# Kernel optimization log

Measured on AMD Instinct MI355X. Metric: run time of the kernel, lower is better.

The kernel has to match this reference:

```python
import jax, jax.numpy as jnp
import numpy as np

D_MODEL = 1024
H = 16
D_K = D_MODEL // H
D_FF = 4096
EPS = 1e-6


def layer_norm(x, alpha, bias):
    mean = jnp.mean(x, axis=-1, keepdims=True)
    var = jnp.mean((x - mean) ** 2, axis=-1, keepdims=True)  # unbiased=False
    return alpha * (x - mean) / jnp.sqrt(var + EPS) + bias


def setup_inputs() -> dict:
    key = jax.random.key(0)
    ks = jax.random.split(key, 8)
    B, S = 4, 2048
    sd = 1.0 / np.sqrt(D_MODEL)
    x = jax.random.normal(ks[0], (B, S, D_MODEL), dtype=jnp.float32)
    src_mask = jnp.ones((B, 1, S), dtype=jnp.int32)
    wq = jax.random.normal(ks[1], (D_MODEL, D_MODEL), jnp.float32) * sd
    wk = jax.random.normal(ks[2], (D_MODEL, D_MODEL), jnp.float32) * sd
    wv = jax.random.normal(ks[3], (D_MODEL, D_MODEL), jnp.float32) * sd
    wo = jax.random.normal(ks[4], (D_MODEL, D_MODEL), jnp.float32) * sd
    w1 = jax.random.normal(ks[5], (D_FF, D_MODEL), jnp.float32) * sd
    b1 = jnp.zeros((D_FF,), jnp.float32)
    w2 = jax.random.normal(ks[6], (D_MODEL, D_FF), jnp.float32) * (1.0 / np.sqrt(D_FF))
    b2 = jnp.zeros((D_MODEL,), jnp.float32)
    ln1_a = jnp.ones((D_MODEL,), jnp.float32)
    ln1_b = jnp.zeros((D_MODEL,), jnp.float32)
    ln2_a = jnp.ones((D_MODEL,), jnp.float32)
    ln2_b = jnp.zeros((D_MODEL,), jnp.float32)
    return dict(x=x, src_mask=src_mask, wq=wq, wk=wk, wv=wv, wo=wo,
                ln1_a=ln1_a, ln1_b=ln1_b, ln2_a=ln2_a, ln2_b=ln2_b,
                w1=w1, b1=b1, w2=w2, b2=b2)


def attention(xn, wq, wk, wv, wo, src_mask):
    B, S, _ = xn.shape
    # torch nn.Linear: y = x @ W.T
    q = (xn @ wq.T).reshape(B, S, H, D_K).transpose(0, 2, 1, 3)  # [B,H,S,Dk]
    k = (xn @ wk.T).reshape(B, S, H, D_K).transpose(0, 2, 1, 3)
    v = (xn @ wv.T).reshape(B, S, H, D_K).transpose(0, 2, 1, 3)
    scores = jnp.einsum('bhqd,bhkd->bhqk', q, k) / np.sqrt(D_K)
    m = src_mask[:, None, :, :]  # [B,1,1,S] from [B,1,S]
    scores = jnp.where(m == 0, -jnp.inf, scores)
    attn = jax.nn.softmax(scores, axis=-1)
    out = jnp.einsum('bhqk,bhkd->bhqd', attn, v)
    out = out.transpose(0, 2, 1, 3).reshape(B, S, D_MODEL)
    return out @ wo.T


def reference(x, src_mask, wq, wk, wv, wo, ln1_a, ln1_b, ln2_a, ln2_b, w1, b1, w2, b2):
    # pre-LN residual 1: self-attention
    xn = layer_norm(x, ln1_a, ln1_b)
    x = x + attention(xn, wq, wk, wv, wo, src_mask)
    # pre-LN residual 2: FFN
    xn = layer_norm(x, ln2_a, ln2_b)
    h = jax.nn.relu(xn @ w1.T + b1)
    x = x + (h @ w2.T + b2)
    return x
```

## Files before the change

### kernel.cpp

```cpp
#include <hip/hip_runtime.h>
#include <stdint.h>

typedef unsigned short u16;
typedef __bf16 bf16x8 __attribute__((ext_vector_type(8)));
typedef float   f32x4 __attribute__((ext_vector_type(4)));
typedef u16     u16x8 __attribute__((ext_vector_type(8)));
typedef u16     u16x4 __attribute__((ext_vector_type(4)));

__device__ __forceinline__ float bf2f(u16 u) {
    union { uint32_t i; float f; } c; c.i = ((uint32_t)u) << 16; return c.f;
}
__device__ __forceinline__ u16 f2bf(float f) {
    union { float f; uint32_t i; } c; c.f = f;
    uint32_t r = c.i + 0x7FFFu + ((c.i >> 16) & 1u);
    return (u16)(r >> 16);
}
__device__ __forceinline__ u16 f2bf_fast(float f) {
    union { float f; uint32_t i; } c; c.f = f;
    return (u16)((c.i + 0x8000u) >> 16);
}
__device__ __forceinline__ uint32_t cvt_pk_bf16(float lo, float hi) {
    uint32_t r;
    asm("v_cvt_pk_bf16_f32 %0, %1, %2" : "=v"(r) : "v"(lo), "v"(hi));
    return r;
}
__device__ __forceinline__ void gload_lds16(const u16* g, u16* l) {
    __builtin_amdgcn_global_load_lds(
        (__attribute__((address_space(1))) void*)(g),
        (__attribute__((address_space(3))) void*)(l), 16, 0, 0);
}

__global__ __launch_bounds__(256) void cvt_all(
    const float* __restrict__ wq, const float* __restrict__ wk,
    const float* __restrict__ wv, const float* __restrict__ wo,
    const float* __restrict__ w1, const float* __restrict__ w2,
    u16* __restrict__ wqb, u16* __restrict__ wkb, u16* __restrict__ wvb,
    u16* __restrict__ wob, u16* __restrict__ w1b, u16* __restrict__ w2b)
{
    int blk = blockIdx.x;
    const float* src; u16* dst; int off;
    if      (blk < 1024)  { src = wq; dst = wqb; off = blk; }
    else if (blk < 2048)  { src = wk; dst = wkb; off = blk - 1024; }
    else if (blk < 3072)  { src = wv; dst = wvb; off = blk - 2048; }
    else if (blk < 4096)  { src = wo; dst = wob; off = blk - 3072; }
    else if (blk < 8192)  { src = w1; dst = w1b; off = blk - 4096; }
    else                  { src = w2; dst = w2b; off = blk - 8192; }
    int i = off * 1024 + threadIdx.x * 4;
    float4 v = *(const float4*)(src + i);
    u16x4 o; o[0] = f2bf(v.x); o[1] = f2bf(v.y); o[2] = f2bf(v.z); o[3] = f2bf(v.w);
    *(u16x4*)(dst + i) = o;
}

__global__ __launch_bounds__(256) void ln_kernel(
    const float* __restrict__ x, const float* __restrict__ ga,
    const float* __restrict__ be, u16* __restrict__ out)
{
    const int D = 1024;
    int row  = blockIdx.x * 4 + (threadIdx.x >> 6);
    int lane = threadIdx.x & 63;
    const float* xr = x + (size_t)row * D + lane * 16;
    float f[16];
#pragma unroll
    for (int i = 0; i < 4; ++i) *(float4*)&f[i * 4] = *(const float4*)(xr + i * 4);
    float s = 0.f, s2 = 0.f;
#pragma unroll
    for (int i = 0; i < 16; ++i) { s += f[i]; s2 += f[i] * f[i]; }
#pragma unroll
    for (int off = 1; off < 64; off <<= 1) {
        s  += __shfl_xor(s,  off, 64);
        s2 += __shfl_xor(s2, off, 64);
    }
    float mean = s * (1.0f / 1024.0f);
    float var  = s2 * (1.0f / 1024.0f) - mean * mean;
    var = var < 0.f ? 0.f : var;
    float inv = 1.0f / sqrtf(var + 1e-6f);
    float g[16], b[16];
#pragma unroll
    for (int i = 0; i < 4; ++i) {
        *(float4*)&g[i * 4] = *(const float4*)(ga + lane * 16 + i * 4);
        *(float4*)&b[i * 4] = *(const float4*)(be + lane * 16 + i * 4);
    }
    u16x8 o0, o1;
#pragma unroll
    for (int i = 0; i < 8; ++i) {
        o0[i] = f2bf(g[i]     * (f[i]     - mean) * inv + b[i]);
        o1[i] = f2bf(g[8 + i] * (f[8 + i] - mean) * inv + b[8 + i]);
    }
    u16* orow = out + (size_t)row * D + lane * 16;
    *(u16x8*)(orow)     = o0;
    *(u16x8*)(orow + 8) = o1;
}

__device__ __forceinline__ void gemm_core(
    const u16* __restrict__ A, const u16* __restrict__ W,
    int K, int ldw, int row_a0, int row_w0,
    u16* As, u16* Bs, f32x4 (&acc)[4][4])
{
    int tid  = threadIdx.x;
    int lane = tid & 63;
    int quad = (lane >> 4), l16 = lane & 15;
    int wave = tid >> 6;
    int wr = wave >> 1, wc = wave & 1;
    int srow = tid >> 2, scol = (tid & 3) * 8;
    const u16* a0p = A + (size_t)(row_a0 + srow) * K + scol;
    const u16* a1p = a0p + (size_t)64 * K;
    const u16* b0p = W + (size_t)(row_w0 + srow) * ldw + scol;
    const u16* b1p = b0p + (size_t)64 * ldw;
    u16* la0 = As + tid * 8;
    u16* la1 = As + 2048 + tid * 8;
    u16* la2 = As + 4096 + tid * 8;
    u16* la3 = As + 6144 + tid * 8;
    u16* lb0 = Bs + tid * 8;
    u16* lb1 = Bs + 2048 + tid * 8;
    u16* lb2 = Bs + 4096 + tid * 8;
    u16* lb3 = Bs + 6144 + tid * 8;

    for (int k0 = 0; k0 < K; k0 += 64) {
        __syncthreads();
        gload_lds16(a0p + k0,      la0);
        gload_lds16(a1p + k0,      la1);
        gload_lds16(a0p + k0 + 32, la2);
        gload_lds16(a1p + k0 + 32, la3);
        gload_lds16(b0p + k0,      lb0);
        gload_lds16(b1p + k0,      lb1);
        gload_lds16(b0p + k0 + 32, lb2);
        gload_lds16(b1p + k0 + 32, lb3);
        __syncthreads();
#pragma unroll
        for (int h = 0; h < 2; ++h) {
            const u16* Ah = As + h * 4096;
            const u16* Bh = Bs + h * 4096;
            bf16x8 af[4], bf[4];
#pragma unroll
            for (int mt = 0; mt < 4; ++mt)
                af[mt] = *(const bf16x8*)(&Ah[(wr * 64 + mt * 16 + l16) * 32 + quad * 8]);
#pragma unroll
            for (int nt = 0; nt < 4; ++nt)
                bf[nt] = *(const bf16x8*)(&Bh[(wc * 64 + nt * 16 + l16) * 32 + quad * 8]);
#pragma unroll
            for (int mt = 0; mt < 4; ++mt)
#pragma unroll
                for (int nt = 0; nt < 4; ++nt)
                    acc[mt][nt] = __builtin_amdgcn_mfma_f32_16x16x32_bf16(
                        af[mt], bf[nt], acc[mt][nt], 0, 0, 0);
        }
    }
}

template<bool OUTF32>
__global__ __launch_bounds__(256) void gemm128(
    const u16* __restrict__ A, const u16* __restrict__ W,
    const float* __restrict__ bias, const float* __restrict__ resid,
    void* __restrict__ Cp, int M, int N, int K, int ldw, int do_relu)
{
    __shared__ u16 As[128 * 64];
    __shared__ u16 Bs[128 * 64];
    int tid  = threadIdx.x;
    int lane = tid & 63, wave = tid >> 6;
    int quad = lane >> 4, l16 = lane & 15;
    int wr = wave >> 1, wc = wave & 1;
    const int row_a0 = blockIdx.x * 128, row_w0 = blockIdx.y * 128;
    f32x4 acc[4][4] = {};
    gemm_core(A, W, K, ldw, row_a0, row_w0, As, Bs, acc);
#pragma unroll
    for (int mt = 0; mt < 4; ++mt) {
#pragma unroll
        for (int nt = 0; nt < 4; ++nt) {
#pragma unroll
            for (int r = 0; r < 4; ++r) {
                int grow = row_a0 + wr * 64 + mt * 16 + quad * 4 + r;
                int gcol = row_w0 + wc * 64 + nt * 16 + l16;
                float vv = acc[mt][nt][r];
                if (bias)    vv += bias[gcol];
                if (do_relu) vv = vv > 0.f ? vv : 0.f;
                if (resid)   vv += resid[(size_t)grow * N + gcol];
                if (OUTF32) ((float*)Cp)[(size_t)grow * N + gcol] = vv;
                else        ((u16*)Cp)[(size_t)grow * N + gcol] = f2bf(vv);
            }
        }
    }
}

__global__ __launch_bounds__(256) void gemm128_qkv(
    const u16* __restrict__ A, const u16* __restrict__ Wqkv,
    u16* __restrict__ qo, u16* __restrict__ ko, u16* __restrict__ vo, int K)
{
    __shared__ u16 As[128 * 64];
    __shared__ u16 Bs[128 * 64];
    int tid  = threadIdx.x;
    int lane = tid & 63, wave = tid >> 6;
    int quad = lane >> 4, l16 = lane & 15;
    int wr = wave >> 1, wc = wave & 1;
    const int row_a0 = blockIdx.x * 128, row_w0 = blockIdx.y * 128;
    f32x4 acc[4][4] = {};
    gemm_core(A, Wqkv, K, K, row_a0, row_w0, As, Bs, acc);
    int seg = row_w0 >> 10;
    u16* dst = (seg == 0) ? qo : (seg == 1) ? ko : vo;
    int col0 = row_w0 & 1023;
#pragma unroll
    for (int mt = 0; mt < 4; ++mt) {
#pragma unroll
        for (int nt = 0; nt < 4; ++nt) {
#pragma unroll
            for (int r = 0; r < 4; ++r) {
                int grow = row_a0 + wr * 64 + mt * 16 + quad * 4 + r;
                int gcol = col0 + wc * 64 + nt * 16 + l16;
                dst[(size_t)grow * 1024 + gcol] = f2bf(acc[mt][nt][r]);
            }
        }
    }
}

__global__ __launch_bounds__(512, 4) void attn_kernel(
    const u16* __restrict__ Q, const u16* __restrict__ Km, const u16* __restrict__ Vm,
    const int* __restrict__ mask, u16* __restrict__ O)
{
    const int S = 2048, DM = 1024;
    const float C1 = 0.18033688f;
    const float C0 = -11.541560f;
    __shared__ u16 smem[35840];
    u16* Ks0 = smem;
    u16* Ks1 = smem + 4096;
    u16* Vt0 = smem + 8192;
    u16* Vt1 = smem + 12800;
    u16* Ps  = smem + 17408;
    u16* Qs  = smem + 17408;

    int qt = blockIdx.x, bh = blockIdx.y;
    int b = bh >> 4, h = bh & 15;
    int tid = threadIdx.x;
    int wave = tid >> 6, lane = tid & 63;
    int quad = lane >> 4, l16 = lane & 15;
    size_t base = (size_t)b * S;
    size_t hoff = (size_t)h * 64;

    {
        int r = tid >> 1, c0 = (tid & 1) * 32;
        const u16* src = Q + (base + qt * 256 + r) * DM + hoff + c0;
        u16* dq = Qs + r * 72 + c0;
        *(u16x8*)(dq)      = *(const u16x8*)(src);
        *(u16x8*)(dq + 8)  = *(const u16x8*)(src + 8);
        *(u16x8*)(dq + 16) = *(const u16x8*)(src + 16);
        *(u16x8*)(dq + 24) = *(const u16x8*)(src + 24);
    }
    const u16* ksrc = Km + (base + (tid >> 3)) * DM + hoff
                    + ((tid & 7) ^ ((tid >> 5) & 7)) * 8;
    int kp = tid & 31, d0 = (tid >> 5) * 4;
    const u16* vsrc = Vm + (base + kp * 2) * DM + hoff + d0;
    const int* msrc = mask + b * S + 4 * l16;

    __syncthreads();
    const int q0 = wave * 32;
    bf16x8 qf00 = *(const bf16x8*)(&Qs[(q0 + l16) * 72 + quad * 8]);
    bf16x8 qf01 = *(const bf16x8*)(&Qs[(q0 + l16) * 72 + 32 + quad * 8]);
    bf16x8 qf10 = *(const bf16x8*)(&Qs[(q0 + 16 + l16) * 72 + quad * 8]);
    bf16x8 qf11 = *(const bf16x8*)(&Qs[(q0 + 16 + l16) * 72 + 32 + quad * 8]);
    const int swz = (l16 & 7) * 8;
    const int u0  = (quad * 8) ^ swz;

    {
        u16x4 va = *(const u16x4*)(vsrc);
        u16x4 vb = *(const u16x4*)(vsrc + DM);
        gload_lds16(ksrc, Ks0 + tid * 8);
        ksrc += 64 * DM; vsrc += 64 * DM;
#pragma unroll
        for (int i = 0; i < 4; ++i) {
            uint32_t w = (uint32_t)va[i] | ((uint32_t)vb[i] << 16);
            *(uint32_t*)(&Vt0[(d0 + i) * 72 + kp * 2]) = w;
        }
    }
    __syncthreads();

    float l0[4] = {0.f, 0.f, 0.f, 0.f};
    float l1[4] = {0.f, 0.f, 0.f, 0.f};
    f32x4 o0[4] = {}, o1[4] = {};

    for (int it = 0; it < 32; ++it) {
        const u16* Kcur = (it & 1) ? Ks1 : Ks0;
        const u16* Vcur = (it & 1) ? Vt1 : Vt0;
        u16* Knxt = (it & 1) ? Ks0 : Ks1;
        u16* Vnxt = (it & 1) ? Vt0 : Vt1;
        const bool pfch = (it < 31);
        u16x4 va, vb;
        if (pfch) {
            va = *(const u16x4*)(vsrc);
            vb = *(const u16x4*)(vsrc + DM);
            gload_lds16(ksrc, Knxt + tid * 8);
            ksrc += 64 * DM; vsrc += 64 * DM;
        }
        f32x4 s0[4] = {}, s1[4] = {};
#pragma unroll
        for (int t = 0; t < 4; ++t) {
            const u16* krp = Kcur + (4 * l16 + t) * 64;
            bf16x8 kf0 = *(const bf16x8*)(krp + u0);
            bf16x8 kf1 = *(const bf16x8*)(krp + (u0 ^ 32));
            s0[t] = __builtin_amdgcn_mfma_f32_16x16x32_bf16(qf00, kf0, s0[t], 0, 0, 0);
            s0[t] = __builtin_amdgcn_mfma_f32_16x16x32_bf16(qf01, kf1, s0[t], 0, 0, 0);
            s1[t] = __builtin_amdgcn_mfma_f32_16x16x32_bf16(qf10, kf0, s1[t], 0, 0, 0);
            s1[t] = __builtin_amdgcn_mfma_f32_16x16x32_bf16(qf11, kf1, s1[t], 0, 0, 0);
        }
        int4 mk4 = *(const int4*)(msrc); msrc += 64;
        float c0t[4];
        c0t[0] = (mk4.x == 0) ? -1e38f : C0;
        c0t[1] = (mk4.y == 0) ? -1e38f : C0;
        c0t[2] = (mk4.z == 0) ? -1e38f : C0;
        c0t[3] = (mk4.w == 0) ? -1e38f : C0;
#pragma unroll
        for (int r = 0; r < 4; ++r) {
            float p0 = exp2f(fmaf(s0[0][r], C1, c0t[0]));
            float p1 = exp2f(fmaf(s0[1][r], C1, c0t[1]));
            float p2 = exp2f(fmaf(s0[2][r], C1, c0t[2]));
            float p3 = exp2f(fmaf(s0[3][r], C1, c0t[3]));
            l0[r] += (p0 + p1) + (p2 + p3);
            uint2 pw;
            pw.x = cvt_pk_bf16(p0, p1);
            pw.y = cvt_pk_bf16(p2, p3);
            *(uint2*)(&Ps[(q0 + quad * 4 + r) * 72 + 4 * l16]) = pw;
        }
#pragma unroll
        for (int r = 0; r < 4; ++r) {
            float p0 = exp2f(fmaf(s1[0][r], C1, c0t[0]));
            float p1 = exp2f(fmaf(s1[1][r], C1, c0t[1]));
            float p2 = exp2f(fmaf(s1[2][r], C1, c0t[2]));
            float p3 = exp2f(fmaf(s1[3][r], C1, c0t[3]));
            l1[r] += (p0 + p1) + (p2 + p3);
            uint2 pw;
            pw.x = cvt_pk_bf16(p0, p1);
            pw.y = cvt_pk_bf16(p2, p3);
            *(uint2*)(&Ps[(q0 + 16 + quad * 4 + r) * 72 + 4 * l16]) = pw;
        }
        bf16x8 pf00 = *(const bf16x8*)(&Ps[(q0 + l16) * 72 + quad * 8]);
        bf16x8 pf01 = *(const bf16x8*)(&Ps[(q0 + l16) * 72 + 32 + quad * 8]);
        bf16x8 pf10 = *(const bf16x8*)(&Ps[(q0 + 16 + l16) * 72 + quad * 8]);
        bf16x8 pf11 = *(const bf16x8*)(&Ps[(q0 + 16 + l16) * 72 + 32 + quad * 8]);
#pragma unroll
        for (int t = 0; t < 4; ++t) {
            bf16x8 vf0 = *(const bf16x8*)(&Vcur[(t * 16 + l16) * 72 + quad * 8]);
            bf16x8 vf1 = *(const bf16x8*)(&Vcur[(t * 16 + l16) * 72 + 32 + quad * 8]);
            o0[t] = __builtin_amdgcn_mfma_f32_16x16x32_bf16(pf00, vf0, o0[t], 0, 0, 0);
            o0[t] = __builtin_amdgcn_mfma_f32_16x16x32_bf16(pf01, vf1, o0[t], 0, 0, 0);
            o1[t] = __builtin_amdgcn_mfma_f32_16x16x32_bf16(pf10, vf0, o1[t], 0, 0, 0);
            o1[t] = __builtin_amdgcn_mfma_f32_16x16x32_bf16(pf11, vf1, o1[t], 0, 0, 0);
        }
        if (pfch) {
#pragma unroll
            for (int i = 0; i < 4; ++i) {
                uint32_t w = (uint32_t)va[i] | ((uint32_t)vb[i] << 16);
                *(uint32_t*)(&Vnxt[(d0 + i) * 72 + kp * 2]) = w;
            }
        }
        __syncthreads();
    }
#pragma unroll
    for (int r = 0; r < 4; ++r) {
#pragma unroll
        for (int off = 1; off < 16; off <<= 1) {
            l0[r] += __shfl_xor(l0[r], off, 16);
            l1[r] += __shfl_xor(l1[r], off, 16);
        }
        float i0 = 1.0f / l0[r];
        float i1 = 1.0f / l1[r];
        u16* dst0 = O + (base + qt * 256 + q0 + quad * 4 + r) * DM + hoff + l16;
        u16* dst1 = dst0 + (size_t)16 * DM;
#pragma unroll
        for (int t = 0; t < 4; ++t) {
            dst0[t * 16] = f2bf(o0[t][r] * i0);
            dst1[t * 16] = f2bf(o1[t][r] * i1);
        }
    }
}

extern "C" void kernel_launch(void* const* d_in, const int* in_sizes, int n_in,
                              void* d_out, int out_size, void* d_ws, size_t ws_size,
                              hipStream_t stream)
{
    (void)in_sizes; (void)n_in; (void)out_size; (void)ws_size;
    const float* x    = (const float*)d_in[0];
    const int*   mask = (const int*)d_in[1];
    const float* wq   = (const float*)d_in[2];
    const float* wk   = (const float*)d_in[3];
    const float* wv   = (const float*)d_in[4];
    const float* wo   = (const float*)d_in[5];
    const float* ln1a = (const float*)d_in[6];
    const float* ln1b = (const float*)d_in[7];
    const float* ln2a = (const float*)d_in[8];
    const float* ln2b = (const float*)d_in[9];
    const float* w1   = (const float*)d_in[10];
    const float* b1   = (const float*)d_in[11];
    const float* w2   = (const float*)d_in[12];
    const float* b2   = (const float*)d_in[13];

    const int M = 8192, D = 1024, F = 4096;
    char* ws = (char*)d_ws;
    u16*  wqkv = (u16*)(ws);
    u16*  wqb = wqkv;
    u16*  wkb = (u16*)(ws + (2u  << 20));
    u16*  wvb = (u16*)(ws + (4u  << 20));
    u16*  wob = (u16*)(ws + (6u  << 20));
    u16*  w1b = (u16*)(ws + (8u  << 20));
    u16*  w2b = (u16*)(ws + (16u << 20));
    u16*  xn  = (u16*)(ws + (24u << 20));
    u16*  q   = (u16*)(ws + (40u << 20));
    u16*  hb  = (u16*)(ws + (40u << 20));

    u16*   kbuf = (u16*)d_out;
    u16*   vbuf = (u16*)d_out + (size_t)M * D;
    float* x1   = (float*)d_out;

    cvt_all<<<12288, 256, 0, stream>>>(wq, wk, wv, wo, w1, w2,
                                       wqb, wkb, wvb, wob, w1b, w2b);

    ln_kernel<<<M / 4, 256, 0, stream>>>(x, ln1a, ln1b, xn);
    dim3 gq(M / 128, 3072 / 128);
    gemm128_qkv<<<gq, 256, 0, stream>>>(xn, wqkv, q, kbuf, vbuf, D);
    dim3 ga(2048 / 256, 64);
    attn_kernel<<<ga, 512, 0, stream>>>(q, kbuf, vbuf, mask, xn);
    dim3 g1(M / 128, D / 128);
    gemm128<true ><<<g1, 256, 0, stream>>>(xn, wob, nullptr, x, x1, M, D, D, D, 0);
    ln_kernel<<<M / 4, 256, 0, stream>>>(x1, ln2a, ln2b, xn);
    dim3 gf1(M / 128, 2048 / 128);
    dim3 gf2(M / 128, D / 128);
    gemm128<false><<<gf1, 256, 0, stream>>>(xn, w1b, b1, nullptr, hb, M, 2048, D, D, 1);
    gemm128<true ><<<gf2, 256, 0, stream>>>(hb, w2b, nullptr, x1, x1, M, D, 2048, F, 0);
    gemm128<false><<<gf1, 256, 0, stream>>>(xn, w1b + (size_t)2048 * D, b1 + 2048, nullptr, hb, M, 2048, D, D, 1);
    gemm128<true ><<<gf2, 256, 0, stream>>>(hb, w2b + 2048, b2, x1, x1, M, D, 2048, F, 0);
}
```

Measured before the change: 620.7 us.

## Widen GEMM tiles to 128x256 with 512 threads and double-buffered LDS

Replaces the 128x128 GEMM with 256 threads by a 128x256 tile computed by 8 waves, and double-buffers the LDS stages so the next K-slice's global-to-LDS loads are issued before the current slice's MFMAs. This is meant to hide global load latency and raise reuse of the A tile across more N columns. In exchange it uses 96KB of LDS per block and halves the number of blocks per GEMM, which lowers the number of blocks available to fill the CUs for the smaller GEMMs. It also removes two unused helper functions.

```diff
diff --git a/kernel.cpp b/kernel.cpp
--- a/kernel.cpp
+++ b/kernel.cpp
@@ -7,17 +7,10 @@
 typedef u16     u16x8 __attribute__((ext_vector_type(8)));
 typedef u16     u16x4 __attribute__((ext_vector_type(4)));
 
-__device__ __forceinline__ float bf2f(u16 u) {
-    union { uint32_t i; float f; } c; c.i = ((uint32_t)u) << 16; return c.f;
-}
 __device__ __forceinline__ u16 f2bf(float f) {
     union { float f; uint32_t i; } c; c.f = f;
     uint32_t r = c.i + 0x7FFFu + ((c.i >> 16) & 1u);
     return (u16)(r >> 16);
-}
-__device__ __forceinline__ u16 f2bf_fast(float f) {
-    union { float f; uint32_t i; } c; c.f = f;
-    return (u16)((c.i + 0x8000u) >> 16);
 }
 __device__ __forceinline__ uint32_t cvt_pk_bf16(float lo, float hi) {
     uint32_t r;
@@ -91,52 +84,62 @@
     *(u16x8*)(orow + 8) = o1;
 }
 
-__device__ __forceinline__ void gemm_core(
+__device__ __forceinline__ void gemm256_core(
     const u16* __restrict__ A, const u16* __restrict__ W,
     int K, int ldw, int row_a0, int row_w0,
-    u16* As, u16* Bs, f32x4 (&acc)[4][4])
+    u16* smem, f32x4 (&acc)[4][4])
 {
     int tid  = threadIdx.x;
     int lane = tid & 63;
-    int quad = (lane >> 4), l16 = lane & 15;
+    int quad = lane >> 4, l16 = lane & 15;
     int wave = tid >> 6;
-    int wr = wave >> 1, wc = wave & 1;
-    int srow = tid >> 2, scol = (tid & 3) * 8;
-    const u16* a0p = A + (size_t)(row_a0 + srow) * K + scol;
-    const u16* a1p = a0p + (size_t)64 * K;
-    const u16* b0p = W + (size_t)(row_w0 + srow) * ldw + scol;
-    const u16* b1p = b0p + (size_t)64 * ldw;
-    u16* la0 = As + tid * 8;
-    u16* la1 = As + 2048 + tid * 8;
-    u16* la2 = As + 4096 + tid * 8;
-    u16* la3 = As + 6144 + tid * 8;
-    u16* lb0 = Bs + tid * 8;
-    u16* lb1 = Bs + 2048 + tid * 8;
-    u16* lb2 = Bs + 4096 + tid * 8;
-    u16* lb3 = Bs + 6144 + tid * 8;
-
-    for (int k0 = 0; k0 < K; k0 += 64) {
-        __syncthreads();
-        gload_lds16(a0p + k0,      la0);
-        gload_lds16(a1p + k0,      la1);
-        gload_lds16(a0p + k0 + 32, la2);
-        gload_lds16(a1p + k0 + 32, la3);
-        gload_lds16(b0p + k0,      lb0);
-        gload_lds16(b1p + k0,      lb1);
-        gload_lds16(b0p + k0 + 32, lb2);
-        gload_lds16(b1p + k0 + 32, lb3);
-        __syncthreads();
+    int wm = wave >> 2, wn = wave & 3;
+
+    const u16* as0 = A + (size_t)(row_a0 + (tid >> 2)) * K   + (tid & 3) * 8;
+    const u16* bs0 = W + (size_t)(row_w0 + (tid >> 2)) * ldw + (tid & 3) * 8;
+    const u16* bs1 = bs0 + (size_t)128 * ldw;
+    u16* d_a0 = smem + tid * 8;
+    u16* d_a1 = smem + 4096  + tid * 8;
+    u16* d_b00 = smem + 8192  + tid * 8;
+    u16* d_b01 = smem + 12288 + tid * 8;
+    u16* d_b10 = smem + 16384 + tid * 8;
+    u16* d_b11 = smem + 20480 + tid * 8;
+
+    const int nk = K >> 6;
+    gload_lds16(as0,      d_a0);
+    gload_lds16(as0 + 32, d_a1);
+    gload_lds16(bs0,      d_b00);
+    gload_lds16(bs0 + 32, d_b10);
+    gload_lds16(bs1,      d_b01);
+    gload_lds16(bs1 + 32, d_b11);
+    __syncthreads();
+
+    const int aoff = (wm * 64 + l16) * 32 + quad * 8;
+    const int boff = (wn * 64 + l16) * 32 + quad * 8;
+
+    for (int t = 0; t < nk; ++t) {
+        const int cb = (t & 1) * 24576;
+        if (t + 1 < nk) {
+            const int nb = ((t + 1) & 1) * 24576;
+            const int k0 = (t + 1) * 64;
+            gload_lds16(as0 + k0,      d_a0  + nb);
+            gload_lds16(as0 + k0 + 32, d_a1  + nb);
+            gload_lds16(bs0 + k0,      d_b00 + nb);
+            gload_lds16(bs0 + k0 + 32, d_b10 + nb);
+            gload_lds16(bs1 + k0,      d_b01 + nb);
+            gload_lds16(bs1 + k0 + 32, d_b11 + nb);
+        }
 #pragma unroll
         for (int h = 0; h < 2; ++h) {
-            const u16* Ah = As + h * 4096;
-            const u16* Bh = Bs + h * 4096;
+            const u16* Ah = smem + cb + h * 4096;
+            const u16* Bh = smem + cb + 8192 + h * 8192;
             bf16x8 af[4], bf[4];
 #pragma unroll
             for (int mt = 0; mt < 4; ++mt)
-                af[mt] = *(const bf16x8*)(&Ah[(wr * 64 + mt * 16 + l16) * 32 + quad * 8]);
+                af[mt] = *(const bf16x8*)(&Ah[aoff + mt * 512]);
 #pragma unroll
             for (int nt = 0; nt < 4; ++nt)
-                bf[nt] = *(const bf16x8*)(&Bh[(wc * 64 + nt * 16 + l16) * 32 + quad * 8]);
+                bf[nt] = *(const bf16x8*)(&Bh[boff + nt * 512]);
 #pragma unroll
             for (int mt = 0; mt < 4; ++mt)
 #pragma unroll
@@ -144,32 +147,32 @@
                     acc[mt][nt] = __builtin_amdgcn_mfma_f32_16x16x32_bf16(
                         af[mt], bf[nt], acc[mt][nt], 0, 0, 0);
         }
+        __syncthreads();
     }
 }
 
 template<bool OUTF32>
-__global__ __launch_bounds__(256) void gemm128(
+__global__ __launch_bounds__(512, 2) void gemm256(
     const u16* __restrict__ A, const u16* __restrict__ W,
     const float* __restrict__ bias, const float* __restrict__ resid,
     void* __restrict__ Cp, int M, int N, int K, int ldw, int do_relu)
 {
-    __shared__ u16 As[128 * 64];
-    __shared__ u16 Bs[128 * 64];
+    __shared__ u16 smem[49152];
     int tid  = threadIdx.x;
     int lane = tid & 63, wave = tid >> 6;
     int quad = lane >> 4, l16 = lane & 15;
-    int wr = wave >> 1, wc = wave & 1;
-    const int row_a0 = blockIdx.x * 128, row_w0 = blockIdx.y * 128;
+    int wm = wave >> 2, wn = wave & 3;
+    const int row_a0 = blockIdx.x * 128, row_w0 = blockIdx.y * 256;
     f32x4 acc[4][4] = {};
-    gemm_core(A, W, K, ldw, row_a0, row_w0, As, Bs, acc);
+    gemm256_core(A, W, K, ldw, row_a0, row_w0, smem, acc);
 #pragma unroll
     for (int mt = 0; mt < 4; ++mt) {
 #pragma unroll
         for (int nt = 0; nt < 4; ++nt) {
 #pragma unroll
             for (int r = 0; r < 4; ++r) {
-                int grow = row_a0 + wr * 64 + mt * 16 + quad * 4 + r;
-                int gcol = row_w0 + wc * 64 + nt * 16 + l16;
+                int grow = row_a0 + wm * 64 + mt * 16 + quad * 4 + r;
+                int gcol = row_w0 + wn * 64 + nt * 16 + l16;
                 float vv = acc[mt][nt][r];
                 if (bias)    vv += bias[gcol];
                 if (do_relu) vv = vv > 0.f ? vv : 0.f;
@@ -181,19 +184,18 @@
     }
 }
 
-__global__ __launch_bounds__(256) void gemm128_qkv(
+__global__ __launch_bounds__(512, 2) void gemm256_qkv(
     const u16* __restrict__ A, const u16* __restrict__ Wqkv,
     u16* __restrict__ qo, u16* __restrict__ ko, u16* __restrict__ vo, int K)
 {
-    __shared__ u16 As[128 * 64];
-    __shared__ u16 Bs[128 * 64];
+    __shared__ u16 smem[49152];
     int tid  = threadIdx.x;
     int lane = tid & 63, wave = tid >> 6;
     int quad = lane >> 4, l16 = lane & 15;
-    int wr = wave >> 1, wc = wave & 1;
-    const int row_a0 = blockIdx.x * 128, row_w0 = blockIdx.y * 128;
+    int wm = wave >> 2, wn = wave & 3;
+    const int row_a0 = blockIdx.x * 128, row_w0 = blockIdx.y * 256;
     f32x4 acc[4][4] = {};
-    gemm_core(A, Wqkv, K, K, row_a0, row_w0, As, Bs, acc);
+    gemm256_core(A, Wqkv, K, K, row_a0, row_w0, smem, acc);
     int seg = row_w0 >> 10;
     u16* dst = (seg == 0) ? qo : (seg == 1) ? ko : vo;
     int col0 = row_w0 & 1023;
@@ -203,8 +205,8 @@
         for (int nt = 0; nt < 4; ++nt) {
 #pragma unroll
             for (int r = 0; r < 4; ++r) {
-                int grow = row_a0 + wr * 64 + mt * 16 + quad * 4 + r;
-                int gcol = col0 + wc * 64 + nt * 16 + l16;
+                int grow = row_a0 + wm * 64 + mt * 16 + quad * 4 + r;
+                int gcol = col0 + wn * 64 + nt * 16 + l16;
                 dst[(size_t)grow * 1024 + gcol] = f2bf(acc[mt][nt][r]);
             }
         }
@@ -411,17 +413,17 @@
                                        wqb, wkb, wvb, wob, w1b, w2b);
 
     ln_kernel<<<M / 4, 256, 0, stream>>>(x, ln1a, ln1b, xn);
-    dim3 gq(M / 128, 3072 / 128);
-    gemm128_qkv<<<gq, 256, 0, stream>>>(xn, wqkv, q, kbuf, vbuf, D);
+    dim3 gq(M / 128, 3072 / 256);
+    gemm256_qkv<<<gq, 512, 0, stream>>>(xn, wqkv, q, kbuf, vbuf, D);
     dim3 ga(2048 / 256, 64);
     attn_kernel<<<ga, 512, 0, stream>>>(q, kbuf, vbuf, mask, xn);
-    dim3 g1(M / 128, D / 128);
-    gemm128<true ><<<g1, 256, 0, stream>>>(xn, wob, nullptr, x, x1, M, D, D, D, 0);
+    dim3 g1(M / 128, D / 256);
+    gemm256<true ><<<g1, 512, 0, stream>>>(xn, wob, nullptr, x, x1, M, D, D, D, 0);
     ln_kernel<<<M / 4, 256, 0, stream>>>(x1, ln2a, ln2b, xn);
-    dim3 gf1(M / 128, 2048 / 128);
-    dim3 gf2(M / 128, D / 128);
-    gemm128<false><<<gf1, 256, 0, stream>>>(xn, w1b, b1, nullptr, hb, M, 2048, D, D, 1);
-    gemm128<true ><<<gf2, 256, 0, stream>>>(hb, w2b, nullptr, x1, x1, M, D, 2048, F, 0);
-    gemm128<false><<<gf1, 256, 0, stream>>>(xn, w1b + (size_t)2048 * D, b1 + 2048, nullptr, hb, M, 2048, D, D, 1);
-    gemm128<true ><<<gf2, 256, 0, stream>>>(hb, w2b + 2048, b2, x1, x1, M, D, 2048, F, 0);
-}
+    dim3 gf1(M / 128, 2048 / 256);
+    dim3 gf2(M / 128, D / 256);
+    gemm256<false><<<gf1, 512, 0, stream>>>(xn, w1b, b1, nullptr, hb, M, 2048, D, D, 1);
+    gemm256<true ><<<gf2, 512, 0, stream>>>(hb, w2b, nullptr, x1, x1, M, D, 2048, F, 0);
+    gemm256<false><<<gf1, 512, 0, stream>>>(xn, w1b + (size_t)2048 * D, b1 + 2048, nullptr, hb, M, 2048, D, D, 1);
+    gemm256<true ><<<gf2, 512, 0, stream>>>(hb, w2b + 2048, b2, x1, x1, M, D, 2048, F, 0);
+}
```

Result: faster. 587.3 us (-5.4%).
